# Optimization experiments

Measured on AMD Instinct MI355X. Metric: run time of the kernel, lower is better.

## Reference

```python
import jax, jax.numpy as jnp
import numpy as np

N = 10000          # nodes
E = 160000         # directed edges (before self loops)
H = 6              # GATConv heads (hardcoded in init_conv)
D = 128            # in_channels = hidden = out_channels
L = 4              # len(hidden_dims) + 1 conv layers
NEG_SLOPE = 0.2    # GATConv default leaky_relu slope


def setup_inputs() -> dict:
    key = jax.random.key(0)
    ks = jax.random.split(key, 2 + 4 * L)
    inp = {}
    inp["x"] = jax.random.normal(ks[0], (N, D), dtype=jnp.float32)
    inp["edge_index"] = jax.random.randint(ks[1], (2, E), 0, N, dtype=jnp.int64)
    for i in range(L):
        kW, ka, kb, kbias = jax.random.split(ks[2 + i], 4)
        scale = 1.0 / np.sqrt(D)
        inp[f"W{i}"] = jax.random.normal(kW, (D, H * D), dtype=jnp.float32) * scale
        inp[f"att_src{i}"] = jax.random.normal(ka, (1, H, D), dtype=jnp.float32) * scale
        inp[f"att_dst{i}"] = jax.random.normal(kb, (1, H, D), dtype=jnp.float32) * scale
        inp[f"b{i}"] = jnp.zeros((D,), dtype=jnp.float32)
    return inp


def _gat_layer(x, src, dst, W, att_src, att_dst, bias):
    # x: [N, Din]; src/dst: [E'] (with self loops); W: [Din, H*C]
    n = x.shape[0]
    xw = (x @ W).reshape(n, H, -1)                      # [N, H, C]
    a_src = jnp.sum(xw * att_src, axis=-1)              # [N, H]
    a_dst = jnp.sum(xw * att_dst, axis=-1)              # [N, H]
    e = jax.nn.leaky_relu(a_src[src] + a_dst[dst], NEG_SLOPE)  # [E', H]
    # segment softmax over edges grouped by destination node
    m = jax.lax.stop_gradient(jax.ops.segment_max(e, dst, num_segments=n))
    e = jnp.exp(e - m[dst])
    denom = jax.ops.segment_sum(e, dst, num_segments=n)  # [N, H]
    alpha = e / (denom[dst] + 1e-16)                     # [E', H]
    out = jax.ops.segment_sum(alpha[:, :, None] * xw[src], dst, num_segments=n)  # [N, H, C]
    return jnp.mean(out, axis=1) + bias                  # concat=False -> head mean


def reference(x, edge_index,
              W0, att_src0, att_dst0, b0,
              W1, att_src1, att_dst1, b1,
              W2, att_src2, att_dst2, b2,
              W3, att_src3, att_dst3, b3):
    n = x.shape[0]
    loops = jnp.arange(n, dtype=edge_index.dtype)
    src = jnp.concatenate([edge_index[0], loops])  # add_self_loops=True
    dst = jnp.concatenate([edge_index[1], loops])
    params = [(W0, att_src0, att_dst0, b0), (W1, att_src1, att_dst1, b1),
              (W2, att_src2, att_dst2, b2), (W3, att_src3, att_dst3, b3)]
    for (W, a_s, a_d, b) in params:
        x = _gat_layer(x, src, dst, W, a_s, a_d, b)
        x = jax.nn.relu(x)  # norm=Identity, dropout eval/no-op; relu applied every layer (jk_mode set)
    return x
```

## Files before the change

kernel.cpp:

```cpp
#include <hip/hip_runtime.h>
#include <hip/hip_fp16.h>
#include <math.h>

#define H 6
#define D 128
#define K_ALL (H * D)
#define TSTEPS 24
#define PADK 776
#define NPB 8
#define BSTRIDE 128

typedef _Float16 f16x8 __attribute__((ext_vector_type(8)));
typedef float f32x4 __attribute__((ext_vector_type(4)));

struct FoldArgs {
    const float* W[4];
    const float* as[4];
    const float* ad[4];
};


__global__ __launch_bounds__(256) void zero_wa_kernel(int4* __restrict__ degz, int n4,
                                                      int zBlocks, FoldArgs fa,
                                                      float* __restrict__ wa_all) {
    int b = blockIdx.x;
    int tid = threadIdx.x;
    if (b < zBlocks) {
        int i = b * 256 + tid;
        if (i < n4) degz[i] = make_int4(0, 0, 0, 0);
        return;
    }
    int t = (b - zBlocks) * 256 + tid;
    if (t >= 4 * 1536) return;
    int l = t / 1536;
    int r = t % 1536;
    int k = r / 12, j = r % 12;
    int h = (j < 6) ? j : (j - 6);
    const float* att = (j < 6) ? fa.as[l] : fa.ad[l];
    const float* wrow = fa.W[l] + (size_t)k * K_ALL + h * D;
    const float* arow = att + h * D;
    float s = 0.f;
    #pragma unroll 8
    for (int c = 0; c < D; c++) s += wrow[c] * arow[c];
    wa_all[(size_t)l * 1536 + k * 12 + j] = s;
}


__global__ __launch_bounds__(256) void prep2_kernel(const int* __restrict__ src,
                                                    const int* __restrict__ dst,
                                                    int* __restrict__ deg,
                                                    int* __restrict__ col, int E,
                                                    int scatBlocks, FoldArgs fa,
                                                    const float* __restrict__ wa_all,
                                                    _Float16* __restrict__ waf,
                                                    _Float16* __restrict__ bf,
                                                    const float* __restrict__ x_in,
                                                    float* __restrict__ a0, int N) {
    __shared__ _Float16 xs[16][136];
    int b = blockIdx.x;
    int tid = threadIdx.x;
    if (b < scatBlocks) {
        int e = b * 256 + tid;
        if (e < E) {
            int n = dst[e];
            int p = atomicAdd(&deg[n], 1);
            if (p < BSTRIDE) col[(size_t)n * BSTRIDE + p] = src[e];
        }
        return;
    }
    int bb = b - scatBlocks;
    if (bb < 192) {
        int idx = bb * 256 + tid;
        int l63 = idx & 63;
        int ct = (idx >> 6) & 7;
        int t = (idx >> 9) % TSTEPS;
        int layer = idx / (TSTEPS * 8 * 64);
        const float* W = fa.W[layer];
        int c = ct * 16 + (l63 & 15);
        f16x8 v;
        #pragma unroll
        for (int j = 0; j < 8; j++) {
            int k = t * 32 + ((l63 >> 4) << 3) + j;
            v[j] = (_Float16)W[(size_t)(k & 127) * K_ALL + ((k >> 7) << 7) + c];
        }
        *(f16x8*)(bf + ((size_t)idx << 3)) = v;
        return;
    }
    bb -= 192;
    if (bb < 4) {
        int L = bb;
        int lane = tid & 63;
        int t = tid >> 6;
        int j = lane & 15;
        const float* wl = wa_all + (size_t)L * 1536;
        f16x8 vv;
        #pragma unroll
        for (int jj = 0; jj < 8; jj++) {
            int k = t * 32 + ((lane >> 4) << 3) + jj;
            float sv = (j < 12) ? wl[k * 12 + j] : 0.f;
            vv[jj] = (_Float16)sv;
        }
        *(f16x8*)(waf + (size_t)L * 2048 + (size_t)t * 512 + (size_t)lane * 8) = vv;
        return;
    }
    bb -= 4;
    int base_node = bb << 4;
    {
        int row = tid >> 4;
        int coff = (tid & 15) * 8;
        int node = base_node + row;
        f16x8 v = {};
        if (node < N) {
            const float* sp = x_in + (size_t)node * D + coff;
            float4 u0 = *(const float4*)sp;
            float4 u1 = *(const float4*)(sp + 4);
            v[0] = (_Float16)u0.x; v[1] = (_Float16)u0.y;
            v[2] = (_Float16)u0.z; v[3] = (_Float16)u0.w;
            v[4] = (_Float16)u1.x; v[5] = (_Float16)u1.y;
            v[6] = (_Float16)u1.z; v[7] = (_Float16)u1.w;
        }
        *(f16x8*)&xs[row][coff] = v;
    }
    __syncthreads();
    if (tid < 64) {
        int lane = tid;
        int cl = lane & 15;
        int r0 = (lane >> 4) << 2;
        const float* wl0 = wa_all;
        f32x4 ac = {0.f, 0.f, 0.f, 0.f};
        #pragma unroll
        for (int t = 0; t < 4; t++) {
            f16x8 av = *(const f16x8*)&xs[cl][t * 32 + ((lane >> 4) << 3)];
            f16x8 bv;
            #pragma unroll
            for (int jj = 0; jj < 8; jj++) {
                int k = t * 32 + ((lane >> 4) << 3) + jj;
                float sv = (cl < 12) ? wl0[k * 12 + cl] : 0.f;
                bv[jj] = (_Float16)sv;
            }
            ac = __builtin_amdgcn_mfma_f32_16x16x32_f16(av, bv, ac, 0, 0, 0);
        }
        if (cl < 12) {
            #pragma unroll
            for (int reg = 0; reg < 4; reg++) {
                int node = base_node + r0 + reg;
                if (node < N) a0[(size_t)node * 12 + cl] = ac[reg];
            }
        }
    }
}

__device__ __forceinline__ float rlf(float v, int j) {
    return __int_as_float(__builtin_amdgcn_readlane(__float_as_int(v), j));
}

__device__ __forceinline__ void aggregate_node(const float* __restrict__ x,
                                               const float* __restrict__ a,
                                               const int* __restrict__ deg_,
                                               const int* __restrict__ col,
                                               int n, int lane,
                                               _Float16* __restrict__ xsrow) {
    const int deg = deg_[n];
    const int start = n << 7;
    const int nent = deg + 1;

    if (nent <= 64) {
        int s = n;
        if (lane < deg) s = col[start + lane];

        const float* xb = x + (lane << 1);
        float2 cur0, cur1, nxt0, nxt1;
        {
            int t0 = __builtin_amdgcn_readlane(s, 0);
            cur0 = *(const float2*)(xb + (size_t)t0 * D);
        }
        cur1 = make_float2(0.f, 0.f);
        nxt0 = make_float2(0.f, 0.f);
        nxt1 = make_float2(0.f, 0.f);
        if (nent > 1) {
            int t1 = __builtin_amdgcn_readlane(s, 1);
            cur1 = *(const float2*)(xb + (size_t)t1 * D);
        }
        if (nent > 2) {
            int t2 = __builtin_amdgcn_readlane(s, 2);
            nxt0 = *(const float2*)(xb + (size_t)t2 * D);
        }
        if (nent > 3) {
            int t3 = __builtin_amdgcn_readlane(s, 3);
            nxt1 = *(const float2*)(xb + (size_t)t3 * D);
        }

        float adst[H];
        #pragma unroll
        for (int h = 0; h < H; h++) adst[h] = a[(size_t)n * 12 + 6 + h];
        const float* as_ = a + (size_t)s * 12;
        float4 v0 = *(const float4*)as_;
        float2 v1 = *(const float2*)(as_ + 4);
        float e0 = v0.x + adst[0], e1 = v0.y + adst[1], e2 = v0.z + adst[2];
        float e3 = v0.w + adst[3], e4 = v1.x + adst[4], e5 = v1.y + adst[5];
        e0 = e0 > 0.f ? e0 : 0.2f * e0;  e1 = e1 > 0.f ? e1 : 0.2f * e1;
        e2 = e2 > 0.f ? e2 : 0.2f * e2;  e3 = e3 > 0.f ? e3 : 0.2f * e3;
        e4 = e4 > 0.f ? e4 : 0.2f * e4;  e5 = e5 > 0.f ? e5 : 0.2f * e5;
        float w0 = __expf(e0), w1 = __expf(e1), w2 = __expf(e2);
        float w3 = __expf(e3), w4 = __expf(e4), w5 = __expf(e5);

        float d0 = 0, d1 = 0, d2 = 0, d3 = 0, d4 = 0, d5 = 0;
        float a00 = 0, a01 = 0, a02 = 0, a03 = 0, a04 = 0, a05 = 0;
        float a10 = 0, a11 = 0, a12 = 0, a13 = 0, a14 = 0, a15 = 0;

        for (int j = 0; j < nent; j += 2) {
            float2 fut0 = make_float2(0.f, 0.f), fut1 = make_float2(0.f, 0.f);
            if (j + 4 < nent) {
                int t = __builtin_amdgcn_readlane(s, j + 4);
                fut0 = *(const float2*)(xb + (size_t)t * D);
            }
            if (j + 5 < nent) {
                int t = __builtin_amdgcn_readlane(s, j + 5);
                fut1 = *(const float2*)(xb + (size_t)t * D);
            }
            {
                float b0 = rlf(w0, j), b1 = rlf(w1, j), b2 = rlf(w2, j);
                float b3 = rlf(w3, j), b4 = rlf(w4, j), b5 = rlf(w5, j);
                d0 += b0; d1 += b1; d2 += b2; d3 += b3; d4 += b4; d5 += b5;
                a00 += b0 * cur0.x; a10 += b0 * cur0.y;
                a01 += b1 * cur0.x; a11 += b1 * cur0.y;
                a02 += b2 * cur0.x; a12 += b2 * cur0.y;
                a03 += b3 * cur0.x; a13 += b3 * cur0.y;
                a04 += b4 * cur0.x; a14 += b4 * cur0.y;
                a05 += b5 * cur0.x; a15 += b5 * cur0.y;
            }
            if (j + 1 < nent) {
                float b0 = rlf(w0, j + 1), b1 = rlf(w1, j + 1), b2 = rlf(w2, j + 1);
                float b3 = rlf(w3, j + 1), b4 = rlf(w4, j + 1), b5 = rlf(w5, j + 1);
                d0 += b0; d1 += b1; d2 += b2; d3 += b3; d4 += b4; d5 += b5;
                a00 += b0 * cur1.x; a10 += b0 * cur1.y;
                a01 += b1 * cur1.x; a11 += b1 * cur1.y;
                a02 += b2 * cur1.x; a12 += b2 * cur1.y;
                a03 += b3 * cur1.x; a13 += b3 * cur1.y;
                a04 += b4 * cur1.x; a14 += b4 * cur1.y;
                a05 += b5 * cur1.x; a15 += b5 * cur1.y;
            }
            cur0 = nxt0; cur1 = nxt1;
            nxt0 = fut0; nxt1 = fut1;
        }
        float i0 = 1.f / d0, i1 = 1.f / d1, i2 = 1.f / d2;
        float i3 = 1.f / d3, i4 = 1.f / d4, i5 = 1.f / d5;
        int c = lane << 1;
        xsrow[0 * D + c] = (_Float16)(a00 * i0);  xsrow[0 * D + c + 1] = (_Float16)(a10 * i0);
        xsrow[1 * D + c] = (_Float16)(a01 * i1);  xsrow[1 * D + c + 1] = (_Float16)(a11 * i1);
        xsrow[2 * D + c] = (_Float16)(a02 * i2);  xsrow[2 * D + c + 1] = (_Float16)(a12 * i2);
        xsrow[3 * D + c] = (_Float16)(a03 * i3);  xsrow[3 * D + c + 1] = (_Float16)(a13 * i3);
        xsrow[4 * D + c] = (_Float16)(a04 * i4);  xsrow[4 * D + c + 1] = (_Float16)(a14 * i4);
        xsrow[5 * D + c] = (_Float16)(a05 * i5);  xsrow[5 * D + c + 1] = (_Float16)(a15 * i5);
    } else {
        float adst[H];
        #pragma unroll
        for (int h = 0; h < H; h++) adst[h] = a[(size_t)n * 12 + 6 + h];
        int dl = deg < BSTRIDE ? deg : BSTRIDE;
        float d[H] = {0, 0, 0, 0, 0, 0};
        float acc0[H] = {0, 0, 0, 0, 0, 0};
        float acc1[H] = {0, 0, 0, 0, 0, 0};
        int c0 = lane, c1 = 64 + lane;
        for (int j = 0; j <= dl; j++) {
            int s = (j < dl) ? col[start + j] : n;
            float w[H];
            #pragma unroll
            for (int h = 0; h < H; h++) {
                float e = a[(size_t)s * 12 + h] + adst[h];
                e = (e > 0.f) ? e : 0.2f * e;
                w[h] = __expf(e);
                d[h] += w[h];
            }
            float xv0 = x[(size_t)s * D + c0];
            float xv1 = x[(size_t)s * D + c1];
            #pragma unroll
            for (int h = 0; h < H; h++) {
                acc0[h] += w[h] * xv0;
                acc1[h] += w[h] * xv1;
            }
        }
        #pragma unroll
        for (int h = 0; h < H; h++) {
            float inv = 1.0f / d[h];
            xsrow[h * D + c0] = (_Float16)(acc0[h] * inv);
            xsrow[h * D + c1] = (_Float16)(acc1[h] * inv);
        }
    }
}

__global__ __launch_bounds__(512) void layer_kernel(const float* __restrict__ x,
                                                    const float* __restrict__ a_in,
                                                    const int* __restrict__ deg_,
                                                    const int* __restrict__ col,
                                                    const _Float16* __restrict__ bf,
                                                    const float* __restrict__ bias,
                                                    float* __restrict__ xout,
                                                    const _Float16* __restrict__ awf,
                                                    float* __restrict__ a_out, int M) {
    __shared__ _Float16 xs16[16][PADK];
    __shared__ _Float16 xso[16][136];
    const int wave = (int)(threadIdx.x >> 6);
    const int lane = (int)(threadIdx.x & 63);
    const int m0 = (int)(blockIdx.x << 3);

    {
        int n = m0 + wave;
        if (n < M)
            aggregate_node(x, a_in, deg_, col, n, lane, &xs16[wave][0]);
    }
    __syncthreads();

    f32x4 acc = {0.f, 0.f, 0.f, 0.f};
    const _Float16* ars = &xs16[lane & 15][(lane >> 4) << 3];
    const _Float16* bp = bf + (size_t)wave * 512 + (size_t)lane * 8;
    for (int t = 0; t < TSTEPS; t++) {
        f16x8 av = *(const f16x8*)(ars + t * 32);
        f16x8 bv = *(const f16x8*)(bp + (size_t)t * 4096);
        acc = __builtin_amdgcn_mfma_f32_16x16x32_f16(av, bv, acc, 0, 0, 0);
    }

    const float inv6 = 1.0f / 6.0f;
    const int cl = lane & 15;
    const int ccol = wave * 16 + cl;
    const int r0 = (lane >> 4) << 2;
    const float bs = bias[ccol];
    #pragma unroll
    for (int reg = 0; reg < 4; reg++) {
        int ml = r0 + reg;
        int m = m0 + ml;
        float v = acc[reg] * inv6 + bs;
        v = v > 0.f ? v : 0.f;
        if (ml < NPB && m < M) xout[(size_t)m * D + ccol] = v;
        xso[ml][ccol] = (_Float16)v;
    }

    if (awf) {
        __syncthreads();
        if (wave == 0) {
            f32x4 ac = {0.f, 0.f, 0.f, 0.f};
            #pragma unroll
            for (int t = 0; t < 4; t++) {
                f16x8 av = *(const f16x8*)&xso[cl][t * 32 + ((lane >> 4) << 3)];
                f16x8 bv = *(const f16x8*)(awf + (size_t)t * 512 + (size_t)lane * 8);
                ac = __builtin_amdgcn_mfma_f32_16x16x32_f16(av, bv, ac, 0, 0, 0);
            }
            if (cl < 12) {
                #pragma unroll
                for (int reg = 0; reg < 4; reg++) {
                    int ml = r0 + reg;
                    int m = m0 + ml;
                    if (ml < NPB && m < M) a_out[(size_t)m * 12 + cl] = ac[reg];
                }
            }
        }
    }
}


extern "C" void kernel_launch(void* const* d_in, const int* in_sizes, int n_in,
                              void* d_out, int out_size, void* d_ws, size_t ws_size,
                              hipStream_t stream) {
    const float* x_in = (const float*)d_in[0];
    const int* ei = (const int*)d_in[1];
    int N = in_sizes[0] / D;
    int E = in_sizes[1] / 2;
    const int* srcp = ei;
    const int* dstp = ei + E;

    size_t bf_halves_per_layer = (size_t)TSTEPS * 8 * 512;

    float* ws = (float*)d_ws;
    float* bufA = ws;
    float* bufB = bufA + (size_t)N * D;
    float* abuf0 = bufB + (size_t)N * D;
    float* abuf1 = abuf0 + (size_t)N * 12;
    float* wa_all = abuf1 + (size_t)N * 12;
    _Float16* waf = (_Float16*)(wa_all + 4 * 1536);
    _Float16* w16f = waf + 4 * 2048;
    int* deg = (int*)(w16f + 4 * bf_halves_per_layer);
    int* col = deg + N;

    FoldArgs fa;
    for (int l = 0; l < 4; l++) {
        fa.W[l]  = (const float*)d_in[2 + 4 * l];
        fa.as[l] = (const float*)d_in[3 + 4 * l];
        fa.ad[l] = (const float*)d_in[4 + 4 * l];
    }

    int n4 = (N + 3) / 4;
    int zBlocks = (n4 + 255) / 256;
    zero_wa_kernel<<<zBlocks + 24, 256, 0, stream>>>((int4*)deg, n4, zBlocks, fa, wa_all);

    int scatBlocks = (E + 255) / 256;
    int a0Blocks = (N + 15) / 16;
    prep2_kernel<<<scatBlocks + 192 + 4 + a0Blocks, 256, 0, stream>>>(
        srcp, dstp, deg, col, E, scatBlocks, fa, wa_all, waf, w16f, x_in, abuf0, N);

    const float* xcur = x_in;
    float* acur = abuf0;
    float* anext = abuf1;
    for (int l = 0; l < 4; l++) {
        const float* b = (const float*)d_in[5 + 4 * l];
        float* xout = (l == 3) ? (float*)d_out : ((l & 1) ? bufB : bufA);
        const _Float16* awf = (l < 3) ? (waf + (size_t)(l + 1) * 2048) : (const _Float16*)nullptr;

        layer_kernel<<<(N + NPB - 1) / NPB, 512, 0, stream>>>(xcur, acur, deg, col,
                                                              w16f + (size_t)l * bf_halves_per_layer,
                                                              b, xout, awf, anext, N);
        xcur = xout;
        float* tmp = acur; acur = anext; anext = tmp;
    }
}
```

Baseline: 130.7 us.

## Merge prep and layer kernels into one cooperative persistent kernel with grid syncs

Replaces the two prep kernels and four per-layer launches with a single cooperative mega-kernel that uses grid-stride loops and grid.sync() between phases. The aim is to remove the per-launch gaps between six dependent kernels. In exchange, the grid is capped at the occupancy limit, so each block loops over several node groups. Grid-wide barriers add their own sync cost, and the prep phases now run with fewer threads in flight.

```diff
diff --git a/kernel.cpp b/kernel.cpp
--- a/kernel.cpp
+++ b/kernel.cpp
@@ -1,6 +1,9 @@
 #include <hip/hip_runtime.h>
 #include <hip/hip_fp16.h>
+#include <hip/hip_cooperative_groups.h>
 #include <math.h>
+
+namespace cg = cooperative_groups;
 
 #define H 6
 #define D 128
@@ -9,146 +12,31 @@
 #define PADK 776
 #define NPB 8
 #define BSTRIDE 128
+#define BF_PL (TSTEPS * 8 * 512)
 
 typedef _Float16 f16x8 __attribute__((ext_vector_type(8)));
 typedef float f32x4 __attribute__((ext_vector_type(4)));
 
-struct FoldArgs {
+struct MegaArgs {
     const float* W[4];
     const float* as[4];
     const float* ad[4];
+    const float* b[4];
+    const float* x_in;
+    const int* src;
+    const int* dst;
+    float* wa_all;
+    _Float16* waf;
+    _Float16* bf;
+    int* deg;
+    int* col;
+    float* a0;
+    float* a1;
+    float* bufA;
+    float* bufB;
+    float* dout;
+    int N, E;
 };
-
-
-__global__ __launch_bounds__(256) void zero_wa_kernel(int4* __restrict__ degz, int n4,
-                                                      int zBlocks, FoldArgs fa,
-                                                      float* __restrict__ wa_all) {
-    int b = blockIdx.x;
-    int tid = threadIdx.x;
-    if (b < zBlocks) {
-        int i = b * 256 + tid;
-        if (i < n4) degz[i] = make_int4(0, 0, 0, 0);
-        return;
-    }
-    int t = (b - zBlocks) * 256 + tid;
-    if (t >= 4 * 1536) return;
-    int l = t / 1536;
-    int r = t % 1536;
-    int k = r / 12, j = r % 12;
-    int h = (j < 6) ? j : (j - 6);
-    const float* att = (j < 6) ? fa.as[l] : fa.ad[l];
-    const float* wrow = fa.W[l] + (size_t)k * K_ALL + h * D;
-    const float* arow = att + h * D;
-    float s = 0.f;
-    #pragma unroll 8
-    for (int c = 0; c < D; c++) s += wrow[c] * arow[c];
-    wa_all[(size_t)l * 1536 + k * 12 + j] = s;
-}
-
-
-__global__ __launch_bounds__(256) void prep2_kernel(const int* __restrict__ src,
-                                                    const int* __restrict__ dst,
-                                                    int* __restrict__ deg,
-                                                    int* __restrict__ col, int E,
-                                                    int scatBlocks, FoldArgs fa,
-                                                    const float* __restrict__ wa_all,
-                                                    _Float16* __restrict__ waf,
-                                                    _Float16* __restrict__ bf,
-                                                    const float* __restrict__ x_in,
-                                                    float* __restrict__ a0, int N) {
-    __shared__ _Float16 xs[16][136];
-    int b = blockIdx.x;
-    int tid = threadIdx.x;
-    if (b < scatBlocks) {
-        int e = b * 256 + tid;
-        if (e < E) {
-            int n = dst[e];
-            int p = atomicAdd(&deg[n], 1);
-            if (p < BSTRIDE) col[(size_t)n * BSTRIDE + p] = src[e];
-        }
-        return;
-    }
-    int bb = b - scatBlocks;
-    if (bb < 192) {
-        int idx = bb * 256 + tid;
-        int l63 = idx & 63;
-        int ct = (idx >> 6) & 7;
-        int t = (idx >> 9) % TSTEPS;
-        int layer = idx / (TSTEPS * 8 * 64);
-        const float* W = fa.W[layer];
-        int c = ct * 16 + (l63 & 15);
-        f16x8 v;
-        #pragma unroll
-        for (int j = 0; j < 8; j++) {
-            int k = t * 32 + ((l63 >> 4) << 3) + j;
-            v[j] = (_Float16)W[(size_t)(k & 127) * K_ALL + ((k >> 7) << 7) + c];
-        }
-        *(f16x8*)(bf + ((size_t)idx << 3)) = v;
-        return;
-    }
-    bb -= 192;
-    if (bb < 4) {
-        int L = bb;
-        int lane = tid & 63;
-        int t = tid >> 6;
-        int j = lane & 15;
-        const float* wl = wa_all + (size_t)L * 1536;
-        f16x8 vv;
-        #pragma unroll
-        for (int jj = 0; jj < 8; jj++) {
-            int k = t * 32 + ((lane >> 4) << 3) + jj;
-            float sv = (j < 12) ? wl[k * 12 + j] : 0.f;
-            vv[jj] = (_Float16)sv;
-        }
-        *(f16x8*)(waf + (size_t)L * 2048 + (size_t)t * 512 + (size_t)lane * 8) = vv;
-        return;
-    }
-    bb -= 4;
-    int base_node = bb << 4;
-    {
-        int row = tid >> 4;
-        int coff = (tid & 15) * 8;
-        int node = base_node + row;
-        f16x8 v = {};
-        if (node < N) {
-            const float* sp = x_in + (size_t)node * D + coff;
-            float4 u0 = *(const float4*)sp;
-            float4 u1 = *(const float4*)(sp + 4);
-            v[0] = (_Float16)u0.x; v[1] = (_Float16)u0.y;
-            v[2] = (_Float16)u0.z; v[3] = (_Float16)u0.w;
-            v[4] = (_Float16)u1.x; v[5] = (_Float16)u1.y;
-            v[6] = (_Float16)u1.z; v[7] = (_Float16)u1.w;
-        }
-        *(f16x8*)&xs[row][coff] = v;
-    }
-    __syncthreads();
-    if (tid < 64) {
-        int lane = tid;
-        int cl = lane & 15;
-        int r0 = (lane >> 4) << 2;
-        const float* wl0 = wa_all;
-        f32x4 ac = {0.f, 0.f, 0.f, 0.f};
-        #pragma unroll
-        for (int t = 0; t < 4; t++) {
-            f16x8 av = *(const f16x8*)&xs[cl][t * 32 + ((lane >> 4) << 3)];
-            f16x8 bv;
-            #pragma unroll
-            for (int jj = 0; jj < 8; jj++) {
-                int k = t * 32 + ((lane >> 4) << 3) + jj;
-                float sv = (cl < 12) ? wl0[k * 12 + cl] : 0.f;
-                bv[jj] = (_Float16)sv;
-            }
-            ac = __builtin_amdgcn_mfma_f32_16x16x32_f16(av, bv, ac, 0, 0, 0);
-        }
-        if (cl < 12) {
-            #pragma unroll
-            for (int reg = 0; reg < 4; reg++) {
-                int node = base_node + r0 + reg;
-                if (node < N) a0[(size_t)node * 12 + cl] = ac[reg];
-            }
-        }
-    }
-}
 
 __device__ __forceinline__ float rlf(float v, int j) {
     return __int_as_float(__builtin_amdgcn_readlane(__float_as_int(v), j));
@@ -288,71 +176,191 @@
     }
 }
 
-__global__ __launch_bounds__(512) void layer_kernel(const float* __restrict__ x,
-                                                    const float* __restrict__ a_in,
-                                                    const int* __restrict__ deg_,
-                                                    const int* __restrict__ col,
-                                                    const _Float16* __restrict__ bf,
-                                                    const float* __restrict__ bias,
-                                                    float* __restrict__ xout,
-                                                    const _Float16* __restrict__ awf,
-                                                    float* __restrict__ a_out, int M) {
+__global__ __launch_bounds__(512) void mega_kernel(MegaArgs A) {
+    cg::grid_group grid = cg::this_grid();
     __shared__ _Float16 xs16[16][PADK];
     __shared__ _Float16 xso[16][136];
-    const int wave = (int)(threadIdx.x >> 6);
-    const int lane = (int)(threadIdx.x & 63);
-    const int m0 = (int)(blockIdx.x << 3);
-
+
+    const int tid = (int)threadIdx.x;
+    const int bid = (int)blockIdx.x;
+    const int gsize = (int)gridDim.x;
+    const long gtid = (long)bid * 512 + tid;
+    const long gthreads = (long)gsize * 512;
+    const int wave = tid >> 6;
+    const int lane = tid & 63;
+    const int N = A.N, E = A.E;
+
+    for (long i = gtid; i < N; i += gthreads) A.deg[i] = 0;
+    for (long t = gtid; t < 4 * 1536; t += gthreads) {
+        int l = (int)(t / 1536);
+        int r = (int)(t % 1536);
+        int k = r / 12, j = r % 12;
+        int h = (j < 6) ? j : (j - 6);
+        const float* att = (j < 6) ? A.as[l] : A.ad[l];
+        const float* wrow = A.W[l] + (size_t)k * K_ALL + h * D;
+        const float* arow = att + h * D;
+        float s = 0.f;
+        #pragma unroll 8
+        for (int c = 0; c < D; c++) s += wrow[c] * arow[c];
+        A.wa_all[(size_t)l * 1536 + k * 12 + j] = s;
+    }
+    grid.sync();
+
+    for (long e = gtid; e < E; e += gthreads) {
+        int n = A.dst[e];
+        int p = atomicAdd(&A.deg[n], 1);
+        if (p < BSTRIDE) A.col[(size_t)n * BSTRIDE + p] = A.src[e];
+    }
+    for (long idx = gtid; idx < 4L * TSTEPS * 8 * 64; idx += gthreads) {
+        int l63 = (int)(idx & 63);
+        int ct = (int)((idx >> 6) & 7);
+        int t = (int)((idx >> 9) % TSTEPS);
+        int layer = (int)(idx / (TSTEPS * 8 * 64));
+        const float* W = A.W[layer];
+        int c = ct * 16 + (l63 & 15);
+        f16x8 v;
+        #pragma unroll
+        for (int j = 0; j < 8; j++) {
+            int k = t * 32 + ((l63 >> 4) << 3) + j;
+            v[j] = (_Float16)W[(size_t)(k & 127) * K_ALL + ((k >> 7) << 7) + c];
+        }
+        *(f16x8*)(A.bf + (idx << 3)) = v;
+    }
+    for (long idx = gtid; idx < 4 * 4 * 64; idx += gthreads) {
+        int L = (int)(idx >> 8);
+        int t = (int)((idx >> 6) & 3);
+        int ln = (int)(idx & 63);
+        int j = ln & 15;
+        const float* wl = A.wa_all + (size_t)L * 1536;
+        f16x8 vv;
+        #pragma unroll
+        for (int jj = 0; jj < 8; jj++) {
+            int k = t * 32 + ((ln >> 4) << 3) + jj;
+            float sv = (j < 12) ? wl[k * 12 + j] : 0.f;
+            vv[jj] = (_Float16)sv;
+        }
+        *(f16x8*)(A.waf + (size_t)L * 2048 + (size_t)t * 512 + (size_t)ln * 8) = vv;
+    }
     {
-        int n = m0 + wave;
-        if (n < M)
-            aggregate_node(x, a_in, deg_, col, n, lane, &xs16[wave][0]);
-    }
-    __syncthreads();
-
-    f32x4 acc = {0.f, 0.f, 0.f, 0.f};
-    const _Float16* ars = &xs16[lane & 15][(lane >> 4) << 3];
-    const _Float16* bp = bf + (size_t)wave * 512 + (size_t)lane * 8;
-    for (int t = 0; t < TSTEPS; t++) {
-        f16x8 av = *(const f16x8*)(ars + t * 32);
-        f16x8 bv = *(const f16x8*)(bp + (size_t)t * 4096);
-        acc = __builtin_amdgcn_mfma_f32_16x16x32_f16(av, bv, acc, 0, 0, 0);
-    }
-
-    const float inv6 = 1.0f / 6.0f;
-    const int cl = lane & 15;
-    const int ccol = wave * 16 + cl;
-    const int r0 = (lane >> 4) << 2;
-    const float bs = bias[ccol];
-    #pragma unroll
-    for (int reg = 0; reg < 4; reg++) {
-        int ml = r0 + reg;
-        int m = m0 + ml;
-        float v = acc[reg] * inv6 + bs;
-        v = v > 0.f ? v : 0.f;
-        if (ml < NPB && m < M) xout[(size_t)m * D + ccol] = v;
-        xso[ml][ccol] = (_Float16)v;
-    }
-
-    if (awf) {
-        __syncthreads();
-        if (wave == 0) {
-            f32x4 ac = {0.f, 0.f, 0.f, 0.f};
+        int G0 = (N + 15) >> 4;
+        for (int g = bid; g < G0; g += gsize) {
+            int base_node = g << 4;
+            if (tid < 256) {
+                int row = tid >> 4;
+                int coff = (tid & 15) * 8;
+                int node = base_node + row;
+                f16x8 v = {};
+                if (node < N) {
+                    const float* sp = A.x_in + (size_t)node * D + coff;
+                    float4 u0 = *(const float4*)sp;
+                    float4 u1 = *(const float4*)(sp + 4);
+                    v[0] = (_Float16)u0.x; v[1] = (_Float16)u0.y;
+                    v[2] = (_Float16)u0.z; v[3] = (_Float16)u0.w;
+                    v[4] = (_Float16)u1.x; v[5] = (_Float16)u1.y;
+                    v[6] = (_Float16)u1.z; v[7] = (_Float16)u1.w;
+                }
+                *(f16x8*)&xso[row][coff] = v;
+            }
+            __syncthreads();
+            if (tid < 64) {
+                int cl = tid & 15;
+                int r0 = (tid >> 4) << 2;
+                const float* wl0 = A.wa_all;
+                f32x4 ac = {0.f, 0.f, 0.f, 0.f};
+                #pragma unroll
+                for (int t = 0; t < 4; t++) {
+                    f16x8 av = *(const f16x8*)&xso[cl][t * 32 + ((tid >> 4) << 3)];
+                    f16x8 bv;
+                    #pragma unroll
+                    for (int jj = 0; jj < 8; jj++) {
+                        int k = t * 32 + ((tid >> 4) << 3) + jj;
+                        float sv = (cl < 12) ? wl0[k * 12 + cl] : 0.f;
+                        bv[jj] = (_Float16)sv;
+                    }
+                    ac = __builtin_amdgcn_mfma_f32_16x16x32_f16(av, bv, ac, 0, 0, 0);
+                }
+                if (cl < 12) {
+                    #pragma unroll
+                    for (int reg = 0; reg < 4; reg++) {
+                        int node = base_node + r0 + reg;
+                        if (node < N) A.a0[(size_t)node * 12 + cl] = ac[reg];
+                    }
+                }
+            }
+            __syncthreads();
+        }
+    }
+    grid.sync();
+
+    const float* xcur = A.x_in;
+    float* acur = A.a0;
+    float* anext = A.a1;
+    const int G = (N + NPB - 1) / NPB;
+    for (int l = 0; l < 4; l++) {
+        const _Float16* bf_l = A.bf + (size_t)l * BF_PL;
+        const float* bias = A.b[l];
+        float* xout = (l == 3) ? A.dout : ((l & 1) ? A.bufB : A.bufA);
+        const _Float16* awf = (l < 3) ? (A.waf + (size_t)(l + 1) * 2048) : (const _Float16*)nullptr;
+
+        for (int g = bid; g < G; g += gsize) {
+            const int m0 = g << 3;
+            {
+                int n = m0 + wave;
+                if (n < N)
+                    aggregate_node(xcur, acur, A.deg, A.col, n, lane, &xs16[wave][0]);
+            }
+            __syncthreads();
+
+            f32x4 acc = {0.f, 0.f, 0.f, 0.f};
+            const _Float16* ars = &xs16[lane & 15][(lane >> 4) << 3];
+            const _Float16* bp = bf_l + (size_t)wave * 512 + (size_t)lane * 8;
+            for (int t = 0; t < TSTEPS; t++) {
+                f16x8 av = *(const f16x8*)(ars + t * 32);
+                f16x8 bv = *(const f16x8*)(bp + (size_t)t * 4096);
+                acc = __builtin_amdgcn_mfma_f32_16x16x32_f16(av, bv, acc, 0, 0, 0);
+            }
+
+            const float inv6 = 1.0f / 6.0f;
+            const int cl = lane & 15;
+            const int ccol = wave * 16 + cl;
+            const int r0 = (lane >> 4) << 2;
+            const float bs = bias[ccol];
             #pragma unroll
-            for (int t = 0; t < 4; t++) {
-                f16x8 av = *(const f16x8*)&xso[cl][t * 32 + ((lane >> 4) << 3)];
-                f16x8 bv = *(const f16x8*)(awf + (size_t)t * 512 + (size_t)lane * 8);
-                ac = __builtin_amdgcn_mfma_f32_16x16x32_f16(av, bv, ac, 0, 0, 0);
-            }
-            if (cl < 12) {
-                #pragma unroll
-                for (int reg = 0; reg < 4; reg++) {
-                    int ml = r0 + reg;
-                    int m = m0 + ml;
-                    if (ml < NPB && m < M) a_out[(size_t)m * 12 + cl] = ac[reg];
+            for (int reg = 0; reg < 4; reg++) {
+                int ml = r0 + reg;
+                int m = m0 + ml;
+                float v = acc[reg] * inv6 + bs;
+                v = v > 0.f ? v : 0.f;
+                if (ml < NPB && m < N) xout[(size_t)m * D + ccol] = v;
+                xso[ml][ccol] = (_Float16)v;
+            }
+
+            if (awf) {
+                __syncthreads();
+                if (wave == 0) {
+                    f32x4 ac = {0.f, 0.f, 0.f, 0.f};
+                    #pragma unroll
+                    for (int t = 0; t < 4; t++) {
+                        f16x8 av = *(const f16x8*)&xso[cl][t * 32 + ((lane >> 4) << 3)];
+                        f16x8 bv = *(const f16x8*)(awf + (size_t)t * 512 + (size_t)lane * 8);
+                        ac = __builtin_amdgcn_mfma_f32_16x16x32_f16(av, bv, ac, 0, 0, 0);
+                    }
+                    if (cl < 12) {
+                        #pragma unroll
+                        for (int reg = 0; reg < 4; reg++) {
+                            int ml = r0 + reg;
+                            int m = m0 + ml;
+                            if (ml < NPB && m < N) anext[(size_t)m * 12 + cl] = ac[reg];
+                        }
+                    }
                 }
             }
-        }
+            __syncthreads();
+        }
+
+        if (l < 3) grid.sync();
+        xcur = xout;
+        float* tmp = acur; acur = anext; anext = tmp;
     }
 }
 
@@ -364,10 +372,6 @@
     const int* ei = (const int*)d_in[1];
     int N = in_sizes[0] / D;
     int E = in_sizes[1] / 2;
-    const int* srcp = ei;
-    const int* dstp = ei + E;
-
-    size_t bf_halves_per_layer = (size_t)TSTEPS * 8 * 512;
 
     float* ws = (float*)d_ws;
     float* bufA = ws;
@@ -377,37 +381,43 @@
     float* wa_all = abuf1 + (size_t)N * 12;
     _Float16* waf = (_Float16*)(wa_all + 4 * 1536);
     _Float16* w16f = waf + 4 * 2048;
-    int* deg = (int*)(w16f + 4 * bf_halves_per_layer);
+    int* deg = (int*)(w16f + 4 * (size_t)BF_PL);
     int* col = deg + N;
 
-    FoldArgs fa;
+    MegaArgs A;
     for (int l = 0; l < 4; l++) {
-        fa.W[l]  = (const float*)d_in[2 + 4 * l];
-        fa.as[l] = (const float*)d_in[3 + 4 * l];
-        fa.ad[l] = (const float*)d_in[4 + 4 * l];
-    }
-
-    int n4 = (N + 3) / 4;
-    int zBlocks = (n4 + 255) / 256;
-    zero_wa_kernel<<<zBlocks + 24, 256, 0, stream>>>((int4*)deg, n4, zBlocks, fa, wa_all);
-
-    int scatBlocks = (E + 255) / 256;
-    int a0Blocks = (N + 15) / 16;
-    prep2_kernel<<<scatBlocks + 192 + 4 + a0Blocks, 256, 0, stream>>>(
-        srcp, dstp, deg, col, E, scatBlocks, fa, wa_all, waf, w16f, x_in, abuf0, N);
-
-    const float* xcur = x_in;
-    float* acur = abuf0;
-    float* anext = abuf1;
-    for (int l = 0; l < 4; l++) {
-        const float* b = (const float*)d_in[5 + 4 * l];
-        float* xout = (l == 3) ? (float*)d_out : ((l & 1) ? bufB : bufA);
-        const _Float16* awf = (l < 3) ? (waf + (size_t)(l + 1) * 2048) : (const _Float16*)nullptr;
-
-        layer_kernel<<<(N + NPB - 1) / NPB, 512, 0, stream>>>(xcur, acur, deg, col,
-                                                              w16f + (size_t)l * bf_halves_per_layer,
-                                                              b, xout, awf, anext, N);
-        xcur = xout;
-        float* tmp = acur; acur = anext; anext = tmp;
-    }
+        A.W[l]  = (const float*)d_in[2 + 4 * l];
+        A.as[l] = (const float*)d_in[3 + 4 * l];
+        A.ad[l] = (const float*)d_in[4 + 4 * l];
+        A.b[l]  = (const float*)d_in[5 + 4 * l];
+    }
+    A.x_in = x_in;
+    A.src = ei;
+    A.dst = ei + E;
+    A.wa_all = wa_all;
+    A.waf = waf;
+    A.bf = w16f;
+    A.deg = deg;
+    A.col = col;
+    A.a0 = abuf0;
+    A.a1 = abuf1;
+    A.bufA = bufA;
+    A.bufB = bufB;
+    A.dout = (float*)d_out;
+    A.N = N;
+    A.E = E;
+
+    int nb = 0;
+    hipOccupancyMaxActiveBlocksPerMultiprocessor(&nb, mega_kernel, 512, 0);
+    if (nb < 1) nb = 1;
+    int dev = 0;
+    hipGetDevice(&dev);
+    int numCU = 256;
+    hipDeviceGetAttribute(&numCU, hipDeviceAttributeMultiprocessorCount, dev);
+    int G = (N + NPB - 1) / NPB;
+    int grid = nb * numCU;
+    if (grid > G) grid = G;
+
+    void* kp[] = { &A };
+    hipLaunchCooperativeKernel((void*)mega_kernel, dim3(grid), dim3(512), kp, 0, stream);
 }
```

New measurement: 379.9 us. 2.91x slower.
